# Performance work log

Hardware: AMD Instinct MI355X
Metric: run time of the kernel (lower is better)

Reference implementation:

```python
import jax, jax.numpy as jnp
import numpy as np
import math

N, D = 8192, 64
KSIZE = 1.0


def setup_inputs() -> dict:
    key = jax.random.key(0)
    kx, kz = jax.random.split(key)
    X = jax.random.normal(kx, (N, D), dtype=jnp.float32)
    Z = jax.random.normal(kz, (N, D), dtype=jnp.float32)
    return {"X": X, "Z": Z}


def _kernel_mean(A, B, ksize):
    # squared pairwise distances via the Gram-matrix expansion instead of
    # materializing the [N, M, D] broadcast diff the torch code implies.
    a2 = jnp.sum(A * A, axis=-1)                      # [N]
    b2 = jnp.sum(B * B, axis=-1)                      # [M]
    d2 = a2[:, None] + b2[None, :] - 2.0 * (A @ B.T)  # [N, M]
    d2 = jnp.maximum(d2, 0.0)                         # numerical guard
    G = jnp.exp(-d2 / ksize) / math.sqrt(2.0 * math.pi * ksize)
    return jnp.mean(G)


def reference(X, Z):
    mxx = _kernel_mean(X, X, KSIZE)
    mzz = _kernel_mean(Z, Z, KSIZE)
    mxz = _kernel_mean(X, Z, KSIZE)
    return jnp.log(jnp.sqrt(mxx * mzz + 1e-5) / (mxz + 1e-5))
```

## Files before the change

### kernel.cpp

```cpp
#include <hip/hip_runtime.h>
#include <hip/hip_bf16.h>
#include <math.h>

#define NN 8192
#define DD 64
#define BJ_MAX 256
#define T1B 4224
#define T2B (2*T1B)
#define TILES_TOTAL 16640
#define NBLOCKS 768
#define EXT_CUT 512
#define NSLOT 32
#define SLOT_STRIDE 16

#define PANEL_ELEMS 1024

typedef __bf16 bf16x8 __attribute__((ext_vector_type(8)));
typedef float f32x4 __attribute__((ext_vector_type(4)));

#if defined(__has_builtin)
#if __has_builtin(__builtin_amdgcn_exp2f)
#define EXP2F __builtin_amdgcn_exp2f
#endif
#endif
#ifndef EXP2F
#define EXP2F exp2f
#endif

#define FMAX3(a,b,c) fmaxf(fmaxf((a),(b)),(c))
#define FMAX4(a,b,c,d) fmaxf(FMAX3((a),(b),(c)),(d))


__global__ __launch_bounds__(256) void prep_kernel(
        const float* __restrict__ X, const float* __restrict__ Z,
        __hip_bfloat16* __restrict__ XbF, __hip_bfloat16* __restrict__ ZbF,
        float* __restrict__ na, float* __restrict__ nb,
        float* __restrict__ partial) {
    int tid = threadIdx.x;
    int gw = blockIdx.x * 4 + (tid >> 6);
    int lane = tid & 63;
    int lm = lane & 15, lk = lane >> 4;
    const float* src = (gw < 512) ? X : Z;
    __hip_bfloat16* dst = (gw < 512) ? XbF : ZbF;
    float* nrm = (gw < 512) ? na : nb;
    int p = (gw < 512) ? gw : gw - 512;
    int row = p * 16 + lm;

    float s = 0.f;
    #pragma unroll
    for (int ks = 0; ks < 2; ++ks) {
        const float4* q = (const float4*)(src + (size_t)row * DD + ks * 32 + lk * 8);
        float4 u = q[0], v = q[1];
        float w[8] = {u.x, u.y, u.z, u.w, v.x, v.y, v.z, v.w};
        unsigned int h[8];
        #pragma unroll
        for (int r = 0; r < 8; ++r) {
            __hip_bfloat16 b = __float2bfloat16(w[r]);
            h[r] = *(unsigned short*)&b;
            float xr = __bfloat162float(b);
            s = fmaf(xr, xr, s);
        }
        uint4 pk;
        pk.x = h[0] | (h[1] << 16); pk.y = h[2] | (h[3] << 16);
        pk.z = h[4] | (h[5] << 16); pk.w = h[6] | (h[7] << 16);
        *(uint4*)(dst + (size_t)p * PANEL_ELEMS + ks * 512 + lane * 8) = pk;
    }
    s += __shfl_xor(s, 16, 64);
    s += __shfl_xor(s, 32, 64);
    if (lk == 0) nrm[row] = -1.4426950408889634f * s;

    if (blockIdx.x == 0) {
        for (int i = tid; i < 3 * NSLOT * SLOT_STRIDE; i += 256) partial[i] = 0.f;
    }
}

__global__ __launch_bounds__(256, 3) void mmd_kernel(
        const __hip_bfloat16* __restrict__ XbFh, const __hip_bfloat16* __restrict__ ZbFh,
        const float* __restrict__ na, const float* __restrict__ nb,
        float* __restrict__ partial) {
    int tid = threadIdx.x;
    int wave = tid >> 6, lane = tid & 63;
    int lm = lane & 15;
    int lk = lane >> 4;
    __shared__ float wsum[4];
    const float C2 = 2.8853900817779268f;
    const int bid = blockIdx.x;
    const bool ext = (bid < EXT_CUT);

    int t0 = bid * 21 + (ext ? bid : EXT_CUT);
    int combo, bi, bj;
    if (t0 < T2B) {
        combo = (t0 < T1B) ? 0 : 1;
        int tt = t0 - (combo ? T1B : 0);
        int rr = (int)((65.0f - sqrtf(4225.0f - (float)tt)) * 0.5f);
        rr = rr < 0 ? 0 : (rr > 31 ? 31 : rr);
        while (rr > 0 && 260 * rr - 4 * rr * rr > tt) --rr;
        while (260 * (rr + 1) - 4 * (rr + 1) * (rr + 1) <= tt) ++rr;
        bi = rr;
        bj = 8 * rr + (tt - (260 * rr - 4 * rr * rr));
    } else {
        combo = 2;
        int rem = t0 - T2B;
        bi = rem >> 8;
        bj = rem & 255;
    }
    const bool sym = (combo != 2);
    const __bf16 *A, *B;
    const float *sa, *sb;
    const __bf16* XbF = (const __bf16*)XbFh;
    const __bf16* ZbF = (const __bf16*)ZbFh;
    if (combo == 0)      { A = XbF; B = XbF; sa = na; sb = na; }
    else if (combo == 1) { A = ZbF; B = ZbF; sa = nb; sb = nb; }
    else                 { A = XbF; B = ZbF; sa = na; sb = nb; }

    bf16x8 af[2][4];
    float nav[4][4], navrtmax[4], navmax;
    {
        int pA = bi * 16 + wave * 4;
        #pragma unroll
        for (int ks = 0; ks < 2; ++ks)
            #pragma unroll
            for (int rt = 0; rt < 4; ++rt)
                af[ks][rt] = *(const bf16x8*)(A + (size_t)(pA + rt) * PANEL_ELEMS + ks * 512 + lane * 8);
        int row0 = bi * 256 + wave * 64;
        #pragma unroll
        for (int rt = 0; rt < 4; ++rt) {
            #pragma unroll
            for (int r = 0; r < 4; ++r) nav[rt][r] = sa[row0 + rt * 16 + lk * 4 + r];
            navrtmax[rt] = FMAX4(nav[rt][0], nav[rt][1], nav[rt][2], nav[rt][3]);
        }
        navmax = FMAX4(navrtmax[0], navrtmax[1], navrtmax[2], navrtmax[3]);
    }

    bf16x8 bufB[2][2][2];
    float bufNb[2][2];
    {
        int pB = bj * 2;
        #pragma unroll
        for (int ks = 0; ks < 2; ++ks)
            #pragma unroll
            for (int ct = 0; ct < 2; ++ct)
                bufB[0][ks][ct] = *(const bf16x8*)(B + (size_t)(pB + ct) * PANEL_ELEMS + ks * 512 + lane * 8);
        int col0 = bj * 32;
        #pragma unroll
        for (int ct = 0; ct < 2; ++ct) bufNb[0][ct] = sb[col0 + ct * 16 + lm];
    }

    float lsum = 0.f;

    #pragma unroll
    for (int it = 0; it < 22; ++it) {
        if (it < 21 || ext) {
            const int cur = it & 1, nxt = cur ^ 1;
            const bool havenext = (it < 20) || (it == 20 && ext);
            int row0 = bi * 256 + wave * 64;
            int col0 = bj * 32;
            bool above = sym && (col0 >= row0 + 64);
            bool elemw = sym && !above;
            float tileScale = above ? 2.f : 1.f;

            int nbi = bi, nbj = bj;
            if (havenext) {
                nbj = bj + 1;
                if (nbj == BJ_MAX) { nbi = bi + 1; nbj = sym ? 8 * nbi : 0; }
                int npB = nbj * 2;
                #pragma unroll
                for (int ks = 0; ks < 2; ++ks)
                    #pragma unroll
                    for (int ct = 0; ct < 2; ++ct)
                        bufB[nxt][ks][ct] = *(const bf16x8*)(B + (size_t)(npB + ct) * PANEL_ELEMS + ks * 512 + lane * 8);
                int ncol0 = nbj * 32;
                #pragma unroll
                for (int ct = 0; ct < 2; ++ct) bufNb[nxt][ct] = sb[ncol0 + ct * 16 + lm];
            }
            __builtin_amdgcn_sched_barrier(0);

            __builtin_amdgcn_s_setprio(1);
            f32x4 acc[4][2] = {};
            #pragma unroll
            for (int ks = 0; ks < 2; ++ks)
                #pragma unroll
                for (int rt = 0; rt < 4; ++rt)
                    #pragma unroll
                    for (int ct = 0; ct < 2; ++ct)
                        acc[rt][ct] = __builtin_amdgcn_mfma_f32_16x16x32_bf16(
                            af[ks][rt], bufB[cur][ks][ct], acc[rt][ct], 0, 0, 0);

            float m00 = FMAX4(acc[0][0][0], acc[0][0][1], acc[0][0][2], acc[0][0][3]);
            float m01 = FMAX4(acc[0][1][0], acc[0][1][1], acc[0][1][2], acc[0][1][3]);
            float m10 = FMAX4(acc[1][0][0], acc[1][0][1], acc[1][0][2], acc[1][0][3]);
            float m11 = FMAX4(acc[1][1][0], acc[1][1][1], acc[1][1][2], acc[1][1][3]);
            float m20 = FMAX4(acc[2][0][0], acc[2][0][1], acc[2][0][2], acc[2][0][3]);
            float m21 = FMAX4(acc[2][1][0], acc[2][1][1], acc[2][1][2], acc[2][1][3]);
            float m30 = FMAX4(acc[3][0][0], acc[3][0][1], acc[3][0][2], acc[3][0][3]);
            float m31 = FMAX4(acc[3][1][0], acc[3][1][1], acc[3][1][2], acc[3][1][3]);
            float gmax = fmaxf(FMAX4(m00, m01, m10, m11), FMAX4(m20, m21, m30, m31));
            __builtin_amdgcn_s_setprio(0);
            float nbmax = fmaxf(bufNb[cur][0], bufNb[cur][1]);
            float tileBound = fmaf(gmax, C2, navmax + nbmax);
            if (__any(tileBound > -30.f)) {
                #pragma unroll
                for (int rt = 0; rt < 4; ++rt) {
                    #pragma unroll
                    for (int ct = 0; ct < 2; ++ct) {
                        float fm = FMAX4(acc[rt][ct][0], acc[rt][ct][1], acc[rt][ct][2], acc[rt][ct][3]);
                        float fb = fmaf(fm, C2, navrtmax[rt] + bufNb[cur][ct]);
                        if (__any(fb > -30.f)) {
                            float base = bufNb[cur][ct];
                            float a0 = fmaf(acc[rt][ct][0], C2, nav[rt][0] + base);
                            float a1 = fmaf(acc[rt][ct][1], C2, nav[rt][1] + base);
                            float a2 = fmaf(acc[rt][ct][2], C2, nav[rt][2] + base);
                            float a3 = fmaf(acc[rt][ct][3], C2, nav[rt][3] + base);
                            float e0 = EXP2F(fminf(a0, 0.f));
                            float e1 = EXP2F(fminf(a1, 0.f));
                            float e2 = EXP2F(fminf(a2, 0.f));
                            float e3 = EXP2F(fminf(a3, 0.f));
                            if (elemw) {
                                int gcol = col0 + ct * 16 + lm;
                                int gr = row0 + rt * 16 + lk * 4;
                                e0 *= (gr + 0 < gcol) ? 2.f : ((gr + 0 == gcol) ? 1.f : 0.f);
                                e1 *= (gr + 1 < gcol) ? 2.f : ((gr + 1 == gcol) ? 1.f : 0.f);
                                e2 *= (gr + 2 < gcol) ? 2.f : ((gr + 2 == gcol) ? 1.f : 0.f);
                                e3 *= (gr + 3 < gcol) ? 2.f : ((gr + 3 == gcol) ? 1.f : 0.f);
                                lsum += (e0 + e1) + (e2 + e3);
                            } else {
                                lsum += tileScale * ((e0 + e1) + (e2 + e3));
                            }
                        }
                    }
                }
            }

            if (havenext && nbi != bi) {
                int npA = nbi * 16 + wave * 4;
                #pragma unroll
                for (int ks = 0; ks < 2; ++ks)
                    #pragma unroll
                    for (int rt = 0; rt < 4; ++rt)
                        af[ks][rt] = *(const bf16x8*)(A + (size_t)(npA + rt) * PANEL_ELEMS + ks * 512 + lane * 8);
                int nrow0 = nbi * 256 + wave * 64;
                #pragma unroll
                for (int rt = 0; rt < 4; ++rt) {
                    #pragma unroll
                    for (int r = 0; r < 4; ++r) nav[rt][r] = sa[nrow0 + rt * 16 + lk * 4 + r];
                    navrtmax[rt] = FMAX4(nav[rt][0], nav[rt][1], nav[rt][2], nav[rt][3]);
                }
                navmax = FMAX4(navrtmax[0], navrtmax[1], navrtmax[2], navrtmax[3]);
                __builtin_amdgcn_sched_barrier(0);
            }
            bi = nbi; bj = nbj;
        }
    }

    #pragma unroll
    for (int off = 32; off; off >>= 1) lsum += __shfl_xor(lsum, off, 64);
    if (lane == 0) wsum[wave] = lsum;
    __syncthreads();
    if (tid == 0) {
        float s = (wsum[0] + wsum[1]) + (wsum[2] + wsum[3]);
        int slot = combo * NSLOT + (bid & (NSLOT - 1));
        atomicAdd(&partial[slot * SLOT_STRIDE], s);
    }
}

__global__ void final_kernel(const float* __restrict__ partial, float* __restrict__ out) {
    __shared__ float s3[3];
    int tid = threadIdx.x;
    if (tid < 3) s3[tid] = 0.f;
    __syncthreads();
    if (tid < 3 * NSLOT) {
        float v = partial[tid * SLOT_STRIDE];
        atomicAdd(&s3[tid / NSLOT], v);
    }
    __syncthreads();
    if (tid == 0) {
        double inv = 1.0 / ((double)NN * (double)NN * 2.5066282746310002);
        double mxx = (double)s3[0] * inv;
        double mzz = (double)s3[1] * inv;
        double mxz = (double)s3[2] * inv;
        double v = log(sqrt(mxx * mzz + 1e-5) / (mxz + 1e-5));
        out[0] = (float)v;
    }
}

extern "C" void kernel_launch(void* const* d_in, const int* in_sizes, int n_in,
                              void* d_out, int out_size, void* d_ws, size_t ws_size,
                              hipStream_t stream) {
    const float* X = (const float*)d_in[0];
    const float* Z = (const float*)d_in[1];
    char* ws = (char*)d_ws;
    __hip_bfloat16* XbF = (__hip_bfloat16*)(ws);
    __hip_bfloat16* ZbF = (__hip_bfloat16*)(ws + 1048576);
    float* na = (float*)(ws + 2097152);
    float* nb = (float*)(ws + 2097152 + 32768);
    float* partial = (float*)(ws + 2097152 + 65536);

    hipLaunchKernelGGL(prep_kernel, dim3(256), dim3(256), 0, stream,
                       X, Z, XbF, ZbF, na, nb, partial);
    hipLaunchKernelGGL(mmd_kernel, dim3(NBLOCKS), dim3(256), 0, stream, XbF, ZbF, na, nb, partial);
    hipLaunchKernelGGL(final_kernel, dim3(1), dim3(128), 0, stream, partial, (float*)d_out);
}
```

Baseline: 30.92 us.

## Software-pipeline MFMA tiles with deferred exp epilogue using double accumulators

Splits each step into an MFMA phase for the current tile and an epilogue (max bound test, exp2, masking, accumulate) for the previous tile, ping-ponging between two accumulator sets. The goal is to let the exp and VALU work of one tile overlap the matrix-core latency of the next. Row-tile maxima are recomputed inside the epilogue instead of being kept live. Holding two accumulator sets raises register pressure and adds bookkeeping to flush the pending tile when the row panel changes and at loop end.

```diff
diff --git a/kernel.cpp b/kernel.cpp
--- a/kernel.cpp
+++ b/kernel.cpp
@@ -114,7 +114,7 @@
     else                 { A = XbF; B = ZbF; sa = na; sb = nb; }
 
     bf16x8 af[2][4];
-    float nav[4][4], navrtmax[4], navmax;
+    float nav[4][4], navmax;
     {
         int pA = bi * 16 + wave * 4;
         #pragma unroll
@@ -124,12 +124,13 @@
                 af[ks][rt] = *(const bf16x8*)(A + (size_t)(pA + rt) * PANEL_ELEMS + ks * 512 + lane * 8);
         int row0 = bi * 256 + wave * 64;
         #pragma unroll
-        for (int rt = 0; rt < 4; ++rt) {
+        for (int rt = 0; rt < 4; ++rt)
             #pragma unroll
             for (int r = 0; r < 4; ++r) nav[rt][r] = sa[row0 + rt * 16 + lk * 4 + r];
-            navrtmax[rt] = FMAX4(nav[rt][0], nav[rt][1], nav[rt][2], nav[rt][3]);
-        }
-        navmax = FMAX4(navrtmax[0], navrtmax[1], navrtmax[2], navrtmax[3]);
+        navmax = fmaxf(fmaxf(FMAX4(nav[0][0], nav[0][1], nav[0][2], nav[0][3]),
+                             FMAX4(nav[1][0], nav[1][1], nav[1][2], nav[1][3])),
+                       fmaxf(FMAX4(nav[2][0], nav[2][1], nav[2][2], nav[2][3]),
+                             FMAX4(nav[3][0], nav[3][1], nav[3][2], nav[3][3])));
     }
 
     bf16x8 bufB[2][2][2];
@@ -147,110 +148,142 @@
     }
 
     float lsum = 0.f;
+    f32x4 accA[4][2], accB[4][2];
+    bool pend = false;
+    int pbi = bi, pbj = bj;
+
+#define EPILOGUE_BODY(ACC, N0, N1)                                                   \
+    {                                                                                \
+        int prow0 = pbi * 256 + wave * 64;                                           \
+        int pcol0 = pbj * 32;                                                        \
+        bool pabove = sym && (pcol0 >= prow0 + 64);                                  \
+        bool pelemw = sym && !pabove;                                                \
+        float pScale = pabove ? 2.f : 1.f;                                           \
+        float m00 = FMAX4(ACC[0][0][0], ACC[0][0][1], ACC[0][0][2], ACC[0][0][3]);   \
+        float m01 = FMAX4(ACC[0][1][0], ACC[0][1][1], ACC[0][1][2], ACC[0][1][3]);   \
+        float m10 = FMAX4(ACC[1][0][0], ACC[1][0][1], ACC[1][0][2], ACC[1][0][3]);   \
+        float m11 = FMAX4(ACC[1][1][0], ACC[1][1][1], ACC[1][1][2], ACC[1][1][3]);   \
+        float m20 = FMAX4(ACC[2][0][0], ACC[2][0][1], ACC[2][0][2], ACC[2][0][3]);   \
+        float m21 = FMAX4(ACC[2][1][0], ACC[2][1][1], ACC[2][1][2], ACC[2][1][3]);   \
+        float m30 = FMAX4(ACC[3][0][0], ACC[3][0][1], ACC[3][0][2], ACC[3][0][3]);   \
+        float m31 = FMAX4(ACC[3][1][0], ACC[3][1][1], ACC[3][1][2], ACC[3][1][3]);   \
+        float gmax = fmaxf(FMAX4(m00, m01, m10, m11), FMAX4(m20, m21, m30, m31));    \
+        float nbmax = fmaxf((N0), (N1));                                             \
+        float tileBound = fmaf(gmax, C2, navmax + nbmax);                            \
+        if (__any(tileBound > -30.f)) {                                              \
+            float pnv[2] = {(N0), (N1)};                                             \
+            float prtmax[4];                                                         \
+            _Pragma("unroll")                                                        \
+            for (int rt = 0; rt < 4; ++rt)                                           \
+                prtmax[rt] = FMAX4(nav[rt][0], nav[rt][1], nav[rt][2], nav[rt][3]);  \
+            _Pragma("unroll")                                                        \
+            for (int rt = 0; rt < 4; ++rt) {                                         \
+                _Pragma("unroll")                                                    \
+                for (int ct = 0; ct < 2; ++ct) {                                     \
+                    float fm = FMAX4(ACC[rt][ct][0], ACC[rt][ct][1], ACC[rt][ct][2], ACC[rt][ct][3]); \
+                    float fb = fmaf(fm, C2, prtmax[rt] + pnv[ct]);                   \
+                    if (__any(fb > -30.f)) {                                         \
+                        float base = pnv[ct];                                        \
+                        float a0 = fmaf(ACC[rt][ct][0], C2, nav[rt][0] + base);      \
+                        float a1 = fmaf(ACC[rt][ct][1], C2, nav[rt][1] + base);      \
+                        float a2 = fmaf(ACC[rt][ct][2], C2, nav[rt][2] + base);      \
+                        float a3 = fmaf(ACC[rt][ct][3], C2, nav[rt][3] + base);      \
+                        float e0 = EXP2F(fminf(a0, 0.f));                            \
+                        float e1 = EXP2F(fminf(a1, 0.f));                            \
+                        float e2 = EXP2F(fminf(a2, 0.f));                            \
+                        float e3 = EXP2F(fminf(a3, 0.f));                            \
+                        if (pelemw) {                                                \
+                            int gcol = pcol0 + ct * 16 + lm;                         \
+                            int gr = prow0 + rt * 16 + lk * 4;                       \
+                            e0 *= (gr + 0 < gcol) ? 2.f : ((gr + 0 == gcol) ? 1.f : 0.f); \
+                            e1 *= (gr + 1 < gcol) ? 2.f : ((gr + 1 == gcol) ? 1.f : 0.f); \
+                            e2 *= (gr + 2 < gcol) ? 2.f : ((gr + 2 == gcol) ? 1.f : 0.f); \
+                            e3 *= (gr + 3 < gcol) ? 2.f : ((gr + 3 == gcol) ? 1.f : 0.f); \
+                            lsum += (e0 + e1) + (e2 + e3);                           \
+                        } else {                                                     \
+                            lsum += pScale * ((e0 + e1) + (e2 + e3));                \
+                        }                                                            \
+                    }                                                                \
+                }                                                                    \
+            }                                                                        \
+        }                                                                            \
+    }
+
+#define STEP_BODY(IT, ACCCUR, ACCPRV)                                                \
+    if ((IT) < 21 || ext) {                                                          \
+        const int cur = (IT) & 1, nxt = cur ^ 1;                                     \
+        const bool havenext = ((IT) < 20) || ((IT) == 20 && ext);                    \
+               \
+        float pn0 = bufNb[nxt][0], pn1 = bufNb[nxt][1];                              \
+        int nbi = bi, nbj = bj;                                                      \
+        if (havenext) {                                                              \
+            nbj = bj + 1;                                                            \
+            if (nbj == BJ_MAX) { nbi = bi + 1; nbj = sym ? 8 * nbi : 0; }            \
+            int npB = nbj * 2;                                                       \
+            _Pragma("unroll")                                                        \
+            for (int ks = 0; ks < 2; ++ks)                                           \
+                for (int ct = 0; ct < 2; ++ct)                                       \
+                    bufB[nxt][ks][ct] = *(const bf16x8*)(B + (size_t)(npB + ct) * PANEL_ELEMS + ks * 512 + lane * 8); \
+            int ncol0 = nbj * 32;                                                    \
+            _Pragma("unroll")                                                        \
+            for (int ct = 0; ct < 2; ++ct) bufNb[nxt][ct] = sb[ncol0 + ct * 16 + lm]; \
+        }                                                                            \
+        __builtin_amdgcn_sched_barrier(0);                                           \
+        __builtin_amdgcn_s_setprio(1);                                               \
+        _Pragma("unroll")                                                            \
+        for (int rt = 0; rt < 4; ++rt)                                               \
+            for (int ct = 0; ct < 2; ++ct)                                           \
+                ACCCUR[rt][ct] = (f32x4){0.f, 0.f, 0.f, 0.f};                        \
+        _Pragma("unroll")                                                            \
+        for (int ks = 0; ks < 2; ++ks)                                               \
+            for (int rt = 0; rt < 4; ++rt)                                           \
+                for (int ct = 0; ct < 2; ++ct)                                       \
+                    ACCCUR[rt][ct] = __builtin_amdgcn_mfma_f32_16x16x32_bf16(        \
+                        af[ks][rt], bufB[cur][ks][ct], ACCCUR[rt][ct], 0, 0, 0);     \
+        __builtin_amdgcn_s_setprio(0);                                               \
+                 \
+        if (pend) EPILOGUE_BODY(ACCPRV, pn0, pn1)                                    \
+                                                   \
+        pbi = bi; pbj = bj; pend = true;                                             \
+        if (havenext) {                                                              \
+            if (nbi != bi) {                                                         \
+                     \
+                EPILOGUE_BODY(ACCCUR, bufNb[cur][0], bufNb[cur][1])                  \
+                pend = false;                                                        \
+                int npA = nbi * 16 + wave * 4;                                       \
+                _Pragma("unroll")                                                    \
+                for (int ks = 0; ks < 2; ++ks)                                       \
+                    for (int rt = 0; rt < 4; ++rt)                                   \
+                        af[ks][rt] = *(const bf16x8*)(A + (size_t)(npA + rt) * PANEL_ELEMS + ks * 512 + lane * 8); \
+                int nrow0 = nbi * 256 + wave * 64;                                   \
+                _Pragma("unroll")                                                    \
+                for (int rt = 0; rt < 4; ++rt)                                       \
+                    for (int r = 0; r < 4; ++r) nav[rt][r] = sa[nrow0 + rt * 16 + lk * 4 + r]; \
+                navmax = fmaxf(fmaxf(FMAX4(nav[0][0], nav[0][1], nav[0][2], nav[0][3]), \
+                                     FMAX4(nav[1][0], nav[1][1], nav[1][2], nav[1][3])), \
+                               fmaxf(FMAX4(nav[2][0], nav[2][1], nav[2][2], nav[2][3]), \
+                                     FMAX4(nav[3][0], nav[3][1], nav[3][2], nav[3][3]))); \
+                __builtin_amdgcn_sched_barrier(0);                                   \
+            }                                                                        \
+            bi = nbi; bj = nbj;                                                      \
+        }                                                                            \
+    }
 
     #pragma unroll
-    for (int it = 0; it < 22; ++it) {
-        if (it < 21 || ext) {
-            const int cur = it & 1, nxt = cur ^ 1;
-            const bool havenext = (it < 20) || (it == 20 && ext);
-            int row0 = bi * 256 + wave * 64;
-            int col0 = bj * 32;
-            bool above = sym && (col0 >= row0 + 64);
-            bool elemw = sym && !above;
-            float tileScale = above ? 2.f : 1.f;
-
-            int nbi = bi, nbj = bj;
-            if (havenext) {
-                nbj = bj + 1;
-                if (nbj == BJ_MAX) { nbi = bi + 1; nbj = sym ? 8 * nbi : 0; }
-                int npB = nbj * 2;
-                #pragma unroll
-                for (int ks = 0; ks < 2; ++ks)
-                    #pragma unroll
-                    for (int ct = 0; ct < 2; ++ct)
-                        bufB[nxt][ks][ct] = *(const bf16x8*)(B + (size_t)(npB + ct) * PANEL_ELEMS + ks * 512 + lane * 8);
-                int ncol0 = nbj * 32;
-                #pragma unroll
-                for (int ct = 0; ct < 2; ++ct) bufNb[nxt][ct] = sb[ncol0 + ct * 16 + lm];
-            }
-            __builtin_amdgcn_sched_barrier(0);
-
-            __builtin_amdgcn_s_setprio(1);
-            f32x4 acc[4][2] = {};
-            #pragma unroll
-            for (int ks = 0; ks < 2; ++ks)
-                #pragma unroll
-                for (int rt = 0; rt < 4; ++rt)
-                    #pragma unroll
-                    for (int ct = 0; ct < 2; ++ct)
-                        acc[rt][ct] = __builtin_amdgcn_mfma_f32_16x16x32_bf16(
-                            af[ks][rt], bufB[cur][ks][ct], acc[rt][ct], 0, 0, 0);
-
-            float m00 = FMAX4(acc[0][0][0], acc[0][0][1], acc[0][0][2], acc[0][0][3]);
-            float m01 = FMAX4(acc[0][1][0], acc[0][1][1], acc[0][1][2], acc[0][1][3]);
-            float m10 = FMAX4(acc[1][0][0], acc[1][0][1], acc[1][0][2], acc[1][0][3]);
-            float m11 = FMAX4(acc[1][1][0], acc[1][1][1], acc[1][1][2], acc[1][1][3]);
-            float m20 = FMAX4(acc[2][0][0], acc[2][0][1], acc[2][0][2], acc[2][0][3]);
-            float m21 = FMAX4(acc[2][1][0], acc[2][1][1], acc[2][1][2], acc[2][1][3]);
-            float m30 = FMAX4(acc[3][0][0], acc[3][0][1], acc[3][0][2], acc[3][0][3]);
-            float m31 = FMAX4(acc[3][1][0], acc[3][1][1], acc[3][1][2], acc[3][1][3]);
-            float gmax = fmaxf(FMAX4(m00, m01, m10, m11), FMAX4(m20, m21, m30, m31));
-            __builtin_amdgcn_s_setprio(0);
-            float nbmax = fmaxf(bufNb[cur][0], bufNb[cur][1]);
-            float tileBound = fmaf(gmax, C2, navmax + nbmax);
-            if (__any(tileBound > -30.f)) {
-                #pragma unroll
-                for (int rt = 0; rt < 4; ++rt) {
-                    #pragma unroll
-                    for (int ct = 0; ct < 2; ++ct) {
-                        float fm = FMAX4(acc[rt][ct][0], acc[rt][ct][1], acc[rt][ct][2], acc[rt][ct][3]);
-                        float fb = fmaf(fm, C2, navrtmax[rt] + bufNb[cur][ct]);
-                        if (__any(fb > -30.f)) {
-                            float base = bufNb[cur][ct];
-                            float a0 = fmaf(acc[rt][ct][0], C2, nav[rt][0] + base);
-                            float a1 = fmaf(acc[rt][ct][1], C2, nav[rt][1] + base);
-                            float a2 = fmaf(acc[rt][ct][2], C2, nav[rt][2] + base);
-                            float a3 = fmaf(acc[rt][ct][3], C2, nav[rt][3] + base);
-                            float e0 = EXP2F(fminf(a0, 0.f));
-                            float e1 = EXP2F(fminf(a1, 0.f));
-                            float e2 = EXP2F(fminf(a2, 0.f));
-                            float e3 = EXP2F(fminf(a3, 0.f));
-                            if (elemw) {
-                                int gcol = col0 + ct * 16 + lm;
-                                int gr = row0 + rt * 16 + lk * 4;
-                                e0 *= (gr + 0 < gcol) ? 2.f : ((gr + 0 == gcol) ? 1.f : 0.f);
-                                e1 *= (gr + 1 < gcol) ? 2.f : ((gr + 1 == gcol) ? 1.f : 0.f);
-                                e2 *= (gr + 2 < gcol) ? 2.f : ((gr + 2 == gcol) ? 1.f : 0.f);
-                                e3 *= (gr + 3 < gcol) ? 2.f : ((gr + 3 == gcol) ? 1.f : 0.f);
-                                lsum += (e0 + e1) + (e2 + e3);
-                            } else {
-                                lsum += tileScale * ((e0 + e1) + (e2 + e3));
-                            }
-                        }
-                    }
-                }
-            }
-
-            if (havenext && nbi != bi) {
-                int npA = nbi * 16 + wave * 4;
-                #pragma unroll
-                for (int ks = 0; ks < 2; ++ks)
-                    #pragma unroll
-                    for (int rt = 0; rt < 4; ++rt)
-                        af[ks][rt] = *(const bf16x8*)(A + (size_t)(npA + rt) * PANEL_ELEMS + ks * 512 + lane * 8);
-                int nrow0 = nbi * 256 + wave * 64;
-                #pragma unroll
-                for (int rt = 0; rt < 4; ++rt) {
-                    #pragma unroll
-                    for (int r = 0; r < 4; ++r) nav[rt][r] = sa[nrow0 + rt * 16 + lk * 4 + r];
-                    navrtmax[rt] = FMAX4(nav[rt][0], nav[rt][1], nav[rt][2], nav[rt][3]);
-                }
-                navmax = FMAX4(navrtmax[0], navrtmax[1], navrtmax[2], navrtmax[3]);
-                __builtin_amdgcn_sched_barrier(0);
-            }
-            bi = nbi; bj = nbj;
+    for (int ii = 0; ii < 11; ++ii) {
+        STEP_BODY(2 * ii,     accA, accB)
+        STEP_BODY(2 * ii + 1, accB, accA)
+    }
+
+    if (pend) {
+        if (ext) {
+            EPILOGUE_BODY(accB, bufNb[1][0], bufNb[1][1])
+        } else {
+            EPILOGUE_BODY(accA, bufNb[0][0], bufNb[0][1])
         }
     }
+#undef STEP_BODY
+#undef EPILOGUE_BODY
 
     #pragma unroll
     for (int off = 32; off; off >>= 1) lsum += __shfl_xor(lsum, off, 64);
```

Measured after the change: 108.7 us. 3.51x slower.
